# Kernel tuning notes

Measured on AMD Instinct MI355X. Metric: run time of the kernel, lower is better.

Reference implementation:

```python
import jax, jax.numpy as jnp
import numpy as np

B, S, N, E = 2048, 5, 80, 592
FX, FF, FE, D = 8, 4, 8, 8
H = 800  # GRU hidden


def setup_inputs() -> dict:
    key = jax.random.key(0)
    ks = jax.random.split(key, 20)
    inp = {
        "x": jax.random.normal(ks[0], (B, S, N, FX), jnp.float32),
        "edge_index": jax.random.randint(ks[1], (B, S, 2, E), 0, N, jnp.int32),
        "edge_f": jax.random.normal(ks[2], (B, S, E, FF), jnp.float32),
        "edge_attr": jax.random.normal(ks[3], (B, S, E, FE), jnp.float32),
        # GNN (net_ResEG) params
        "Wx": jax.random.normal(ks[4], (FX, D), jnp.float32) * 0.1,
        "We": jax.random.normal(ks[5], (FE, D), jnp.float32) * 0.1,
        "Wf": jax.random.normal(ks[6], (FF, D), jnp.float32) * 0.1,
        "Wedge": jax.random.normal(ks[7], (2 * D + FE, D), jnp.float32) * 0.1,
        # GRU params (PyTorch layout: [3H, in])
        "w_ih": jax.random.normal(ks[8], (3 * H, N * D + E * D), jnp.float32) * 0.02,
        "w_hh": jax.random.normal(ks[9], (3 * H, H), jnp.float32) * 0.02,
        "b_ih": jnp.zeros((3 * H,), jnp.float32),
        "b_hh": jnp.zeros((3 * H,), jnp.float32),
        # MLP params
        "mlp_w1": jax.random.normal(ks[10], (S * H, 1280), jnp.float32) * 0.02,
        "mlp_b1": jnp.zeros((1280,), jnp.float32),
        "mlp_w2": jax.random.normal(ks[11], (1280, S * 80), jnp.float32) * 0.02,
        "mlp_b2": jnp.zeros((S * 80,), jnp.float32),
    }
    return inp


def _gnn(xg, eig, efg, eag, Wx, We, Wf, Wedge):
    # one graph: xg [N,FX], eig [2,E], efg [E,FF], eag [E,FE]
    src, dst = eig[0], eig[1]
    m = jax.nn.relu(eag @ We + efg @ Wf)            # [E,D] edge messages
    agg = jnp.zeros((N, D), m.dtype).at[dst].add(m)  # scatter-add to nodes
    x_out = xg + jax.nn.relu(xg @ Wx + agg)          # residual node update [N,D]
    feat = jnp.concatenate([x_out[src], x_out[dst], eag], axis=-1)  # [E,2D+FE]
    e_out = eag + jax.nn.relu(feat @ Wedge)          # residual edge update [E,D]
    return x_out, e_out


def _forward(x, edge_index, edge_f, edge_attr, Wx, We, Wf, Wedge,
             w_ih, w_hh, b_ih, b_hh, mlp_w1, mlp_b1, mlp_w2, mlp_b2):
    # normalize edge indices (edge_index[i,j] - edge_index[i,j,0].min())
    mins = edge_index[:, :, 0, :].min(axis=-1)[:, :, None, None]  # [B,S,1,1]
    ei = edge_index - mins

    flat = lambda a: a.reshape((B * S,) + a.shape[2:])
    x1, e1 = jax.vmap(lambda a, b, c, d: _gnn(a, b, c, d, Wx, We, Wf, Wedge))(
        flat(x), flat(ei), flat(edge_f), flat(edge_attr))
    x1 = x1.reshape(B, S, N * D)
    e1 = e1.reshape(B, S, E * D)
    seq = jnp.concatenate([x1, e1], axis=2)  # [B,S,5376]

    # single-layer GRU, batch_first (dropout inactive for 1 layer)
    def step(h, xt):
        gi = xt @ w_ih.T + b_ih   # [B,3H]
        gh = h @ w_hh.T + b_hh
        ir, iz, inn = jnp.split(gi, 3, axis=-1)
        hr, hz, hn = jnp.split(gh, 3, axis=-1)
        r = jax.nn.sigmoid(ir + hr)
        z = jax.nn.sigmoid(iz + hz)
        n = jnp.tanh(inn + r * hn)
        h_new = (1.0 - z) * n + z * h
        return h_new, h_new

    h0 = jnp.zeros((B, H), seq.dtype)
    _, ys = jax.lax.scan(step, h0, jnp.swapaxes(seq, 0, 1))  # [S,B,H]
    y = jnp.swapaxes(ys, 0, 1).reshape(B, S * H)             # [B,4000]

    y = y @ mlp_w1 + mlp_b1
    y = y @ mlp_w2 + mlp_b2
    return y.reshape(B, 80, 5)


def reference(x, edge_index, edge_f, edge_attr, Wx, We, Wf, Wedge,
              w_ih, w_hh, b_ih, b_hh, mlp_w1, mlp_b1, mlp_w2, mlp_b2):
    return _forward(x, edge_index, edge_f, edge_attr, Wx, We, Wf, Wedge,
                    w_ih, w_hh, b_ih, b_hh, mlp_w1, mlp_b1, mlp_w2, mlp_b2)
```

## Files before the change

kernel.cpp:

```cpp
#include <hip/hip_runtime.h>
#include <math.h>

constexpr int B_  = 2048;
constexpr int S_  = 5;
constexpr int N_  = 80;
constexpr int E_  = 592;
constexpr int FX_ = 8;
constexpr int FF_ = 4;
constexpr int FE_ = 8;
constexpr int D_  = 8;
constexpr int H_  = 800;

constexpr int BS_  = B_ * S_;
constexpr int XD_  = N_ * D_;
constexpr int ED_  = E_ * D_;
constexpr int SEQ_ = XD_ + ED_;
constexpr int G3_  = 3 * H_;
constexpr int MIN_ = S_ * H_;
constexpr int MH_  = 1280;
constexpr int MO_  = S_ * 80;

typedef __bf16 bf16_t;
typedef __bf16 bf16x8 __attribute__((ext_vector_type(8)));
typedef float  f32x4  __attribute__((ext_vector_type(4)));

__device__ __forceinline__ float sigmoidf_(float x) {
    return 1.0f / (1.0f + expf(-x));
}

__device__ __forceinline__ void async16(const void* g, void* l) {
    __builtin_amdgcn_global_load_lds(
        (const __attribute__((address_space(1))) unsigned int*)g,
        (__attribute__((address_space(3))) unsigned int*)l,
        16, 0, 0);
}

__global__ __launch_bounds__(256) void gnn_kernel(
    const float* __restrict__ x,
    const int*   __restrict__ ei,
    const float* __restrict__ ef,
    const float* __restrict__ ea,
    const float* __restrict__ Wx,
    const float* __restrict__ We,
    const float* __restrict__ Wf,
    const float* __restrict__ Wedge,
    bf16_t* __restrict__ seq)
{
    const int g   = blockIdx.x;
    const int tid = threadIdx.x;

    __shared__ float sWx[FX_ * D_];
    __shared__ float sWe[FE_ * D_];
    __shared__ float sWf[FF_ * D_];
    __shared__ float sWedge[24 * D_];
    __shared__ float agg[N_ * D_];
    __shared__ float xout[N_ * D_];
    __shared__ int   s_src[E_];
    __shared__ int   s_dst[E_];
    __shared__ int   s_min;

    if (tid == 0) s_min = 0x7fffffff;
    if (tid < FX_ * D_) sWx[tid] = Wx[tid];
    if (tid < FE_ * D_) sWe[tid] = We[tid];
    if (tid < FF_ * D_) sWf[tid] = Wf[tid];
    if (tid < 24 * D_)  sWedge[tid] = Wedge[tid];
    for (int i = tid; i < N_ * D_; i += 256) agg[i] = 0.0f;
    __syncthreads();

    const int* srcp = ei + (size_t)g * 2 * E_;
    const int* dstp = srcp + E_;
    int lmin = 0x7fffffff;
    for (int e = tid; e < E_; e += 256) {
        int sv = srcp[e];
        int dv = dstp[e];
        s_src[e] = sv;
        s_dst[e] = dv;
        lmin = min(lmin, sv);
    }
    atomicMin(&s_min, lmin);
    __syncthreads();
    const int mn = s_min;

    const float* eag = ea + (size_t)g * E_ * FE_;
    const float* efg = ef + (size_t)g * E_ * FF_;
    for (int e = tid; e < E_; e += 256) {
        float a[FE_], f[FF_];
        const float4* ap = (const float4*)(eag + (size_t)e * FE_);
        float4 a0 = ap[0], a1 = ap[1];
        a[0]=a0.x; a[1]=a0.y; a[2]=a0.z; a[3]=a0.w;
        a[4]=a1.x; a[5]=a1.y; a[6]=a1.z; a[7]=a1.w;
        float4 f0 = *(const float4*)(efg + (size_t)e * FF_);
        f[0]=f0.x; f[1]=f0.y; f[2]=f0.z; f[3]=f0.w;

        int dadj = s_dst[e] - mn;
        if (dadj < 0) dadj += N_;

        #pragma unroll
        for (int d = 0; d < D_; d++) {
            float m = 0.0f;
            #pragma unroll
            for (int k = 0; k < FE_; k++) m += a[k] * sWe[k * D_ + d];
            #pragma unroll
            for (int k = 0; k < FF_; k++) m += f[k] * sWf[k * D_ + d];
            m = fmaxf(m, 0.0f);
            atomicAdd(&agg[dadj * D_ + d], m);
        }
    }
    __syncthreads();

    const float* xg = x + (size_t)g * N_ * FX_;
    bf16_t* seqrow = seq + (size_t)g * SEQ_;
    for (int n = tid; n < N_; n += 256) {
        float xi[FX_];
        const float4* xp = (const float4*)(xg + (size_t)n * FX_);
        float4 x0 = xp[0], x1 = xp[1];
        xi[0]=x0.x; xi[1]=x0.y; xi[2]=x0.z; xi[3]=x0.w;
        xi[4]=x1.x; xi[5]=x1.y; xi[6]=x1.z; xi[7]=x1.w;
        #pragma unroll
        for (int d = 0; d < D_; d++) {
            float v = agg[n * D_ + d];
            #pragma unroll
            for (int k = 0; k < FX_; k++) v += xi[k] * sWx[k * D_ + d];
            v = fmaxf(v, 0.0f);
            float o = xi[d] + v;
            xout[n * D_ + d] = o;
            seqrow[n * D_ + d] = (bf16_t)o;
        }
    }
    __syncthreads();

    for (int e = tid; e < E_; e += 256) {
        int sadj = s_src[e] - mn;
        int dadj = s_dst[e] - mn;
        if (dadj < 0) dadj += N_;
        float a[FE_];
        const float4* ap = (const float4*)(eag + (size_t)e * FE_);
        float4 a0 = ap[0], a1 = ap[1];
        a[0]=a0.x; a[1]=a0.y; a[2]=a0.z; a[3]=a0.w;
        a[4]=a1.x; a[5]=a1.y; a[6]=a1.z; a[7]=a1.w;
        const float* xs = &xout[sadj * D_];
        const float* xd = &xout[dadj * D_];
        #pragma unroll
        for (int d = 0; d < D_; d++) {
            float v = 0.0f;
            #pragma unroll
            for (int k = 0; k < D_; k++)  v += xs[k] * sWedge[k * D_ + d];
            #pragma unroll
            for (int k = 0; k < D_; k++)  v += xd[k] * sWedge[(D_ + k) * D_ + d];
            #pragma unroll
            for (int k = 0; k < FE_; k++) v += a[k] * sWedge[(2 * D_ + k) * D_ + d];
            v = fmaxf(v, 0.0f);
            seqrow[XD_ + e * D_ + d] = (bf16_t)(a[d] + v);
        }
    }
}

template <typename OutT>
__global__ __launch_bounds__(256) void mfma_gemm_bt(
    const bf16_t* __restrict__ A,
    const bf16_t* __restrict__ Bm,
    const float*  __restrict__ bias,
    OutT* __restrict__ C,
    int M, int Nn, int K)
{
    __shared__ bf16_t As[128 * 32];
    __shared__ bf16_t Bs[128 * 32];

    const int tid  = threadIdx.x;
    const int wave = tid >> 6;
    const int lane = tid & 63;
    const int m0 = blockIdx.y * 128;
    const int n0 = blockIdx.x * 128;
    const int wm = (wave & 1) * 64;
    const int wn = (wave >> 1) * 64;

    const int srow  = tid >> 2;
    const int skoff = (tid & 3) * 8;

    const int fm = lane & 15;
    const int fk = (lane >> 4) * 8;

    f32x4 acc[4][4] = {};

    const bf16_t* a_ptr0 = A + (size_t)(m0 + srow) * K + skoff;
    const bf16_t* a_ptr1 = a_ptr0 + (size_t)64 * K;
    int brow0 = n0 + srow;      if (brow0 > Nn - 1) brow0 = Nn - 1;
    int brow1 = n0 + 64 + srow; if (brow1 > Nn - 1) brow1 = Nn - 1;
    const bf16_t* b_ptr0 = Bm + (size_t)brow0 * K + skoff;
    const bf16_t* b_ptr1 = Bm + (size_t)brow1 * K + skoff;

    bf16_t* lA0 = &As[srow * 32 + skoff];
    bf16_t* lA1 = &As[(64 + srow) * 32 + skoff];
    bf16_t* lB0 = &Bs[srow * 32 + skoff];
    bf16_t* lB1 = &Bs[(64 + srow) * 32 + skoff];

    for (int k0 = 0; k0 < K; k0 += 32) {
        async16(a_ptr0 + k0, lA0);
        async16(a_ptr1 + k0, lA1);
        async16(b_ptr0 + k0, lB0);
        async16(b_ptr1 + k0, lB1);
        __syncthreads();

        bf16x8 af[4], bfm[4];
        #pragma unroll
        for (int i = 0; i < 4; i++)
            af[i] = *(const bf16x8*)&As[(wm + i * 16 + fm) * 32 + fk];
        #pragma unroll
        for (int j = 0; j < 4; j++)
            bfm[j] = *(const bf16x8*)&Bs[(wn + j * 16 + fm) * 32 + fk];

        #pragma unroll
        for (int i = 0; i < 4; i++)
            #pragma unroll
            for (int j = 0; j < 4; j++)
                acc[i][j] = __builtin_amdgcn_mfma_f32_16x16x32_bf16(
                    af[i], bfm[j], acc[i][j], 0, 0, 0);

        __syncthreads();
    }

    const int crow = (lane >> 4) * 4;
    const int ccol = lane & 15;
    #pragma unroll
    for (int i = 0; i < 4; i++) {
        #pragma unroll
        for (int j = 0; j < 4; j++) {
            int row = m0 + wm + i * 16 + crow;
            int col = n0 + wn + j * 16 + ccol;
            if (col < Nn) {
                float bv = bias[col];
                #pragma unroll
                for (int r = 0; r < 4; r++) {
                    float v = acc[i][j][r] + bv;
                    C[(size_t)(row + r) * Nn + col] = (OutT)v;
                }
            }
        }
    }
}

__global__ __launch_bounds__(256) void f2bf_kernel(
    const float* __restrict__ in, bf16_t* __restrict__ out, int n)
{
    int i = (blockIdx.x * 256 + threadIdx.x) * 4;
    if (i + 3 < n) {
        float4 v = *(const float4*)&in[i];
        out[i + 0] = (bf16_t)v.x;
        out[i + 1] = (bf16_t)v.y;
        out[i + 2] = (bf16_t)v.z;
        out[i + 3] = (bf16_t)v.w;
    } else {
        for (; i < n; i++) out[i] = (bf16_t)in[i];
    }
}

__global__ __launch_bounds__(256) void tconv_kernel(
    const float* __restrict__ in, bf16_t* __restrict__ out, int K, int N)
{
    __shared__ float tile[32][33];
    int k0 = blockIdx.y * 32, n0 = blockIdx.x * 32;
    int tx = threadIdx.x & 31, ty = threadIdx.x >> 5;
    #pragma unroll
    for (int r = 0; r < 32; r += 8) {
        int k = k0 + ty + r, n = n0 + tx;
        tile[ty + r][tx] = (k < K && n < N) ? in[(size_t)k * N + n] : 0.0f;
    }
    __syncthreads();
    #pragma unroll
    for (int r = 0; r < 32; r += 8) {
        int n = n0 + ty + r, k = k0 + tx;
        if (n < N && k < K) out[(size_t)n * K + k] = (bf16_t)tile[tx][ty + r];
    }
}

__global__ __launch_bounds__(256) void gru_gates_kernel(
    const float* __restrict__ gi,
    const float* __restrict__ gh,
    float*  __restrict__ h,
    bf16_t* __restrict__ hb,
    bf16_t* __restrict__ yb,
    int t)
{
    int i = blockIdx.x * blockDim.x + threadIdx.x;
    if (i >= B_ * H_) return;
    int b = i / H_;
    int j = i - b * H_;
    const float* girow = gi + ((size_t)b * S_ + t) * G3_;
    const float* ghrow = gh + (size_t)b * G3_;
    float r = sigmoidf_(girow[j] + ghrow[j]);
    float z = sigmoidf_(girow[H_ + j] + ghrow[H_ + j]);
    float n = tanhf(girow[2 * H_ + j] + r * ghrow[2 * H_ + j]);
    float hp = h[i];
    float hn = (1.0f - z) * n + z * hp;
    h[i] = hn;
    hb[i] = (bf16_t)hn;
    yb[(size_t)b * MIN_ + t * H_ + j] = (bf16_t)hn;
}

extern "C" void kernel_launch(void* const* d_in, const int* in_sizes, int n_in,
                              void* d_out, int out_size, void* d_ws, size_t ws_size,
                              hipStream_t stream) {
    const float* x     = (const float*)d_in[0];
    const int*   ei    = (const int*)  d_in[1];
    const float* ef    = (const float*)d_in[2];
    const float* ea    = (const float*)d_in[3];
    const float* Wx    = (const float*)d_in[4];
    const float* We    = (const float*)d_in[5];
    const float* Wf    = (const float*)d_in[6];
    const float* Wedge = (const float*)d_in[7];
    const float* w_ih  = (const float*)d_in[8];
    const float* w_hh  = (const float*)d_in[9];
    const float* b_ih  = (const float*)d_in[10];
    const float* b_hh  = (const float*)d_in[11];
    const float* w1    = (const float*)d_in[12];
    const float* b1    = (const float*)d_in[13];
    const float* w2    = (const float*)d_in[14];
    const float* b2    = (const float*)d_in[15];
    float* out = (float*)d_out;

    char* p = (char*)d_ws;
    auto alloc = [&](size_t bytes) {
        void* r = (void*)p;
        p += (bytes + 255) & ~(size_t)255;
        return r;
    };
    bf16_t* seq   = (bf16_t*)alloc((size_t)BS_ * SEQ_ * 2);
    bf16_t* wihb  = (bf16_t*)alloc((size_t)G3_ * SEQ_ * 2);
    bf16_t* whhb  = (bf16_t*)alloc((size_t)G3_ * H_ * 2);
    bf16_t* w1t   = (bf16_t*)alloc((size_t)MH_ * MIN_ * 2);
    bf16_t* w2t   = (bf16_t*)alloc((size_t)MO_ * MH_ * 2);
    float*  gi    = (float*) alloc((size_t)BS_ * G3_ * 4);
    float*  gh    = (float*) alloc((size_t)B_ * G3_ * 4);
    float*  h     = (float*) alloc((size_t)B_ * H_ * 4);
    bf16_t* hb    = (bf16_t*)alloc((size_t)B_ * H_ * 2);
    bf16_t* yb    = (bf16_t*)alloc((size_t)B_ * MIN_ * 2);
    bf16_t* t1b   = (bf16_t*)alloc((size_t)B_ * MH_ * 2);

    hipMemsetAsync(h,  0, (size_t)B_ * H_ * sizeof(float), stream);
    hipMemsetAsync(hb, 0, (size_t)B_ * H_ * sizeof(bf16_t), stream);

    {
        int n = G3_ * SEQ_;
        f2bf_kernel<<<(n / 4 + 255) / 256, 256, 0, stream>>>(w_ih, wihb, n);
    }
    {
        int n = G3_ * H_;
        f2bf_kernel<<<(n / 4 + 255) / 256, 256, 0, stream>>>(w_hh, whhb, n);
    }
    {
        dim3 grid((MH_ + 31) / 32, (MIN_ + 31) / 32);
        tconv_kernel<<<grid, 256, 0, stream>>>(w1, w1t, MIN_, MH_);
    }
    {
        dim3 grid((MO_ + 31) / 32, (MH_ + 31) / 32);
        tconv_kernel<<<grid, 256, 0, stream>>>(w2, w2t, MH_, MO_);
    }

    gnn_kernel<<<BS_, 256, 0, stream>>>(x, ei, ef, ea, Wx, We, Wf, Wedge, seq);

    {
        dim3 grid((G3_ + 127) / 128, BS_ / 128);
        mfma_gemm_bt<float><<<grid, 256, 0, stream>>>(seq, wihb, b_ih, gi, BS_, G3_, SEQ_);
    }

    for (int t = 0; t < S_; t++) {
        dim3 grid((G3_ + 127) / 128, B_ / 128);
        mfma_gemm_bt<float><<<grid, 256, 0, stream>>>(hb, whhb, b_hh, gh, B_, G3_, H_);
        gru_gates_kernel<<<(B_ * H_ + 255) / 256, 256, 0, stream>>>(gi, gh, h, hb, yb, t);
    }

    {
        dim3 grid((MH_ + 127) / 128, B_ / 128);
        mfma_gemm_bt<bf16_t><<<grid, 256, 0, stream>>>(yb, w1t, b1, t1b, B_, MH_, MIN_);
    }
    {
        dim3 grid((MO_ + 127) / 128, B_ / 128);
        mfma_gemm_bt<float><<<grid, 256, 0, stream>>>(t1b, w2t, b2, out, B_, MO_, MH_);
    }
}
```

Baseline: 1.554 ms.

## Process one graph per wavefront in GNN kernel with wave-level sync

```diff
diff --git a/kernel.cpp b/kernel.cpp
--- a/kernel.cpp
+++ b/kernel.cpp
@@ -35,7 +35,13 @@
         16, 0, 0);
 }
 
-__global__ __launch_bounds__(256) void gnn_kernel(
+__device__ __forceinline__ void wave_sync() {
+    __builtin_amdgcn_wave_barrier();
+    __asm__ volatile("s_waitcnt lgkmcnt(0)" ::: "memory");
+    __builtin_amdgcn_wave_barrier();
+}
+
+__global__ __launch_bounds__(256, 5) void gnn_kernel(
     const float* __restrict__ x,
     const int*   __restrict__ ei,
     const float* __restrict__ ef,
@@ -46,44 +52,53 @@
     const float* __restrict__ Wedge,
     bf16_t* __restrict__ seq)
 {
-    const int g   = blockIdx.x;
-    const int tid = threadIdx.x;
+    const int tid  = threadIdx.x;
+    const int w    = tid >> 6;
+    const int lane = tid & 63;
+    const int g    = blockIdx.x * 4 + w;
 
     __shared__ float sWx[FX_ * D_];
     __shared__ float sWe[FE_ * D_];
     __shared__ float sWf[FF_ * D_];
     __shared__ float sWedge[24 * D_];
-    __shared__ float agg[N_ * D_];
-    __shared__ float xout[N_ * D_];
-    __shared__ int   s_src[E_];
-    __shared__ int   s_dst[E_];
-    __shared__ int   s_min;
-
-    if (tid == 0) s_min = 0x7fffffff;
+    __shared__ float agg[4][D_ * N_];
+    __shared__ float xout[4][N_ * D_];
+    __shared__ unsigned char esrc[4][E_];
+    __shared__ unsigned char edst[4][E_];
+
     if (tid < FX_ * D_) sWx[tid] = Wx[tid];
     if (tid < FE_ * D_) sWe[tid] = We[tid];
     if (tid < FF_ * D_) sWf[tid] = Wf[tid];
     if (tid < 24 * D_)  sWedge[tid] = Wedge[tid];
-    for (int i = tid; i < N_ * D_; i += 256) agg[i] = 0.0f;
     __syncthreads();
+
+    float* aggw  = agg[w];
+    float* xoutw = xout[w];
+    unsigned char* srcw = esrc[w];
+    unsigned char* dstw = edst[w];
+
+    #pragma unroll
+    for (int i = 0; i < 10; i++) aggw[i * 64 + lane] = 0.0f;
 
     const int* srcp = ei + (size_t)g * 2 * E_;
     const int* dstp = srcp + E_;
     int lmin = 0x7fffffff;
-    for (int e = tid; e < E_; e += 256) {
+    for (int e = lane; e < E_; e += 64) {
         int sv = srcp[e];
         int dv = dstp[e];
-        s_src[e] = sv;
-        s_dst[e] = dv;
+        srcw[e] = (unsigned char)sv;
+        dstw[e] = (unsigned char)dv;
         lmin = min(lmin, sv);
     }
-    atomicMin(&s_min, lmin);
-    __syncthreads();
-    const int mn = s_min;
+    #pragma unroll
+    for (int m = 1; m < 64; m <<= 1)
+        lmin = min(lmin, __shfl_xor(lmin, m));
+    const int mn = lmin;
+    wave_sync();
 
     const float* eag = ea + (size_t)g * E_ * FE_;
     const float* efg = ef + (size_t)g * E_ * FF_;
-    for (int e = tid; e < E_; e += 256) {
+    for (int e = lane; e < E_; e += 64) {
         float a[FE_], f[FF_];
         const float4* ap = (const float4*)(eag + (size_t)e * FE_);
         float4 a0 = ap[0], a1 = ap[1];
@@ -92,7 +107,7 @@
         float4 f0 = *(const float4*)(efg + (size_t)e * FF_);
         f[0]=f0.x; f[1]=f0.y; f[2]=f0.z; f[3]=f0.w;
 
-        int dadj = s_dst[e] - mn;
+        int dadj = (int)dstw[e] - mn;
         if (dadj < 0) dadj += N_;
 
         #pragma unroll
@@ -103,43 +118,50 @@
             #pragma unroll
             for (int k = 0; k < FF_; k++) m += f[k] * sWf[k * D_ + d];
             m = fmaxf(m, 0.0f);
-            atomicAdd(&agg[dadj * D_ + d], m);
+            atomicAdd(&aggw[d * N_ + dadj], m);
         }
     }
-    __syncthreads();
+    wave_sync();
 
     const float* xg = x + (size_t)g * N_ * FX_;
     bf16_t* seqrow = seq + (size_t)g * SEQ_;
-    for (int n = tid; n < N_; n += 256) {
+    for (int n = lane; n < N_; n += 64) {
         float xi[FX_];
         const float4* xp = (const float4*)(xg + (size_t)n * FX_);
         float4 x0 = xp[0], x1 = xp[1];
         xi[0]=x0.x; xi[1]=x0.y; xi[2]=x0.z; xi[3]=x0.w;
         xi[4]=x1.x; xi[5]=x1.y; xi[6]=x1.z; xi[7]=x1.w;
+        bf16x8 o;
         #pragma unroll
         for (int d = 0; d < D_; d++) {
-            float v = agg[n * D_ + d];
+            float v = aggw[d * N_ + n];
             #pragma unroll
             for (int k = 0; k < FX_; k++) v += xi[k] * sWx[k * D_ + d];
             v = fmaxf(v, 0.0f);
-            float o = xi[d] + v;
-            xout[n * D_ + d] = o;
-            seqrow[n * D_ + d] = (bf16_t)o;
+            float ov = xi[d] + v;
+            xoutw[n * D_ + d] = ov;
+            o[d] = (bf16_t)ov;
         }
-    }
-    __syncthreads();
-
-    for (int e = tid; e < E_; e += 256) {
-        int sadj = s_src[e] - mn;
-        int dadj = s_dst[e] - mn;
+        *(bf16x8*)&seqrow[n * D_] = o;
+    }
+    wave_sync();
+
+    for (int e = lane; e < E_; e += 64) {
+        int sadj = (int)srcw[e] - mn;
+        int dadj = (int)dstw[e] - mn;
         if (dadj < 0) dadj += N_;
         float a[FE_];
         const float4* ap = (const float4*)(eag + (size_t)e * FE_);
         float4 a0 = ap[0], a1 = ap[1];
         a[0]=a0.x; a[1]=a0.y; a[2]=a0.z; a[3]=a0.w;
         a[4]=a1.x; a[5]=a1.y; a[6]=a1.z; a[7]=a1.w;
-        const float* xs = &xout[sadj * D_];
-        const float* xd = &xout[dadj * D_];
+        float4 xs0 = *(const float4*)&xoutw[sadj * D_];
+        float4 xs1 = *(const float4*)&xoutw[sadj * D_ + 4];
+        float4 xd0 = *(const float4*)&xoutw[dadj * D_];
+        float4 xd1 = *(const float4*)&xoutw[dadj * D_ + 4];
+        float xs[D_] = {xs0.x,xs0.y,xs0.z,xs0.w,xs1.x,xs1.y,xs1.z,xs1.w};
+        float xd[D_] = {xd0.x,xd0.y,xd0.z,xd0.w,xd1.x,xd1.y,xd1.z,xd1.w};
+        bf16x8 o;
         #pragma unroll
         for (int d = 0; d < D_; d++) {
             float v = 0.0f;
@@ -150,8 +172,9 @@
             #pragma unroll
             for (int k = 0; k < FE_; k++) v += a[k] * sWedge[(2 * D_ + k) * D_ + d];
             v = fmaxf(v, 0.0f);
-            seqrow[XD_ + e * D_ + d] = (bf16_t)(a[d] + v);
+            o[d] = (bf16_t)(a[d] + v);
         }
+        *(bf16x8*)&seqrow[XD_ + e * D_] = o;
     }
 }
 
@@ -356,7 +379,7 @@
         tconv_kernel<<<grid, 256, 0, stream>>>(w2, w2t, MH_, MO_);
     }
 
-    gnn_kernel<<<BS_, 256, 0, stream>>>(x, ei, ef, ea, Wx, We, Wf, Wedge, seq);
+    gnn_kernel<<<BS_ / 4, 256, 0, stream>>>(x, ei, ef, ea, Wx, We, Wf, Wedge, seq);
 
     {
         dim3 grid((G3_ + 127) / 128, BS_ / 128);
```

Measured after the change: 1.981 ms. 27.4% more time.
